# Kernel tuning notes

Hardware: AMD Instinct MI355X
Metric: run time of the kernel (lower is better)

Reference implementation:

```python
import jax, jax.numpy as jnp
import numpy as np

D_MODEL = 1024
NUM_HEADS = 16
D_K = D_MODEL // NUM_HEADS
B, N = 4, 2048


def setup_inputs() -> dict:
    key = jax.random.key(0)
    ks = jax.random.split(key, 5)
    scale = 1.0 / np.sqrt(D_MODEL)
    return {
        "x": jax.random.normal(ks[0], (B, N, D_MODEL), dtype=jnp.float32),
        "wq": jax.random.normal(ks[1], (D_MODEL, D_MODEL), dtype=jnp.float32) * scale,
        "wk": jax.random.normal(ks[2], (D_MODEL, D_MODEL), dtype=jnp.float32) * scale,
        "wv": jax.random.normal(ks[3], (D_MODEL, D_MODEL), dtype=jnp.float32) * scale,
        "wo": jax.random.normal(ks[4], (D_MODEL, D_MODEL), dtype=jnp.float32) * scale,
    }


def reference(x, wq, wk, wv, wo):
    b, n, d = x.shape
    # torch Linear(weight W) computes x @ W.T
    def proj(w):
        return (x @ w.T).reshape(b, n, NUM_HEADS, D_K).transpose(0, 2, 1, 3)  # [B,H,N,d_k]
    Q, K, V = proj(wq), proj(wk), proj(wv)
    scores = jnp.einsum("bhqd,bhkd->bhqk", Q, K) / jnp.sqrt(jnp.float32(D_K))
    causal = jnp.tril(jnp.ones((n, n), dtype=bool))
    scores = jnp.where(causal, scores, jnp.float32(-jnp.inf))
    attn = jax.nn.softmax(scores, axis=-1)
    vals = jnp.einsum("bhqk,bhkd->bhqd", attn, V)  # [B,H,N,d_k]
    vals = vals.transpose(0, 2, 1, 3).reshape(b, n, d)
    out = vals @ wo.T
    return (out, K, V)
```

## Files before the change

### kernel.cpp

```cpp
#include <hip/hip_runtime.h>
#include <hip/hip_bf16.h>

typedef __bf16 bf16_t;
typedef __bf16 bf16x8 __attribute__((ext_vector_type(8)));
typedef __bf16 bf16x4 __attribute__((ext_vector_type(4)));
typedef float f32x4 __attribute__((ext_vector_type(4)));
typedef float f32x16 __attribute__((ext_vector_type(16)));
typedef int i32x4 __attribute__((ext_vector_type(4)));

#define LDS_AS __attribute__((address_space(3)))
#define GLB_AS __attribute__((address_space(1)))

__device__ __forceinline__ void gload_lds16(const void* g, void* l) {
  __builtin_amdgcn_global_load_lds((const GLB_AS void*)g, (LDS_AS void*)l, 16, 0, 0);
}

static __device__ __forceinline__ f32x4 mfma16(bf16x8 a, bf16x8 b, f32x4 c) {
  return __builtin_amdgcn_mfma_f32_16x16x32_bf16(a, b, c, 0, 0, 0);
}
static __device__ __forceinline__ f32x16 mfma32(bf16x8 a, bf16x8 b, f32x16 c) {
  return __builtin_amdgcn_mfma_f32_32x32x16_bf16(a, b, c, 0, 0, 0);
}
__device__ __forceinline__ int cvtpk_bf16(float lo, float hi) {
  int r;
  asm("v_cvt_pk_bf16_f32 %0, %1, %2" : "=v"(r) : "v"(lo), "v"(hi));
  return r;
}
__device__ __forceinline__ bf16x8 mkfrag(int w0, int w1, int w2, int w3) {
  i32x4 v;
  v[0] = w0; v[1] = w1; v[2] = w2; v[3] = w3;
  return __builtin_bit_cast(bf16x8, v);
}

#define PIPE_WAIT_BARRIER(N)                                   \
  asm volatile("s_waitcnt vmcnt(" #N ")" ::: "memory");        \
  __builtin_amdgcn_s_barrier();                                \
  asm volatile("" ::: "memory");                               \
  __builtin_amdgcn_sched_barrier(0)

#define PIPE_END_BARRIER()                                     \
  __builtin_amdgcn_s_barrier();                                \
  asm volatile("" ::: "memory");                               \
  __builtin_amdgcn_sched_barrier(0)

#define QSCALE 0.18033688011112042f

__global__ __launch_bounds__(256) void cast_kernel(
    const float* __restrict__ x, const float* __restrict__ wq,
    const float* __restrict__ wk, const float* __restrict__ wv,
    const float* __restrict__ wo, bf16_t* __restrict__ xb,
    bf16_t* __restrict__ wqb, bf16_t* __restrict__ wkb,
    bf16_t* __restrict__ wvb, bf16_t* __restrict__ wob) {
  size_t i = ((size_t)blockIdx.x * 256 + threadIdx.x) * 4;
  const float* s;
  bf16_t* d;
  size_t off;
  if (i < 8388608) {
    s = x; d = xb; off = i;
  } else {
    size_t j = i - 8388608;
    int wi = (int)(j >> 20);
    off = j & 1048575;
    s = wi == 0 ? wq : wi == 1 ? wk : wi == 2 ? wv : wo;
    d = wi == 0 ? wqb : wi == 1 ? wkb : wi == 2 ? wvb : wob;
  }
  float4 v = *(const float4*)(s + off);
  bf16x4 o;
  o[0] = (bf16_t)v.x; o[1] = (bf16_t)v.y; o[2] = (bf16_t)v.z; o[3] = (bf16_t)v.w;
  *(bf16x4*)(d + off) = o;
}

__global__ __launch_bounds__(512) void gemm_qkv(
    const bf16_t* __restrict__ xb, const bf16_t* __restrict__ wqb,
    const bf16_t* __restrict__ wkb, const bf16_t* __restrict__ wvb,
    bf16_t* __restrict__ Qb, bf16_t* __restrict__ Kb, bf16_t* __restrict__ vTb,
    float* __restrict__ outK, float* __restrict__ outV) {
  __shared__ __align__(16) bf16_t lds[32768];
  const int tid = threadIdx.x;
  const int lane = tid & 63, w = tid >> 6;
  const int llo = lane & 15, lhi = lane >> 4;
  const int wm = w >> 2, wn = w & 3;
  const int rowBase = blockIdx.x * 128, colW = blockIdx.y * 128;

  const int arow = tid >> 2, asrc = (tid & 3) ^ ((arow >> 1) & 3);
  const bf16_t* srcA = xb + (size_t)(rowBase + arow) * 1024 + asrc * 8;
  const bf16_t* srcB0 = wqb + (size_t)(colW + arow) * 1024 + asrc * 8;
  const bf16_t* srcB1 = wkb + (size_t)(colW + arow) * 1024 + asrc * 8;
  const bf16_t* srcB2 = wvb + (size_t)(colW + arow) * 1024 + asrc * 8;
  const int dstA = tid * 8;
  const int dstB0 = 4096 + tid * 8;
  const int dstB1 = 4096 + (512 + tid) * 8;
  const int dstB2 = 4096 + (1024 + tid) * 8;

  auto STAGE = [&](int kt, int b) {
    bf16_t* base = lds + b * 16384;
    gload_lds16(srcA + kt * 32, base + dstA);
    gload_lds16(srcB0 + kt * 32, base + dstB0);
    gload_lds16(srcB1 + kt * 32, base + dstB1);
    gload_lds16(srcB2 + kt * 32, base + dstB2);
  };

  f32x4 acc[4][6] = {};
  const int xr = (llo >> 1) & 3;
  STAGE(0, 0);
  for (int kt = 0; kt < 32; ++kt) {
    if (kt + 1 < 32) {
      STAGE(kt + 1, (kt + 1) & 1);
      PIPE_WAIT_BARRIER(4);
    } else {
      PIPE_WAIT_BARRIER(0);
    }
    const bf16_t* bufA = lds + (kt & 1) * 16384;
    const bf16_t* bufB = bufA + 4096;
    bf16x8 aF[4], bF[6];
#pragma unroll
    for (int mf = 0; mf < 4; ++mf)
      aF[mf] = *(const bf16x8*)&bufA[(wm * 64 + mf * 16 + llo) * 32 +
                                     ((lhi ^ xr) * 8)];
#pragma unroll
    for (int nf = 0; nf < 6; ++nf)
      bF[nf] = *(const bf16x8*)&bufB[(wn * 96 + nf * 16 + llo) * 32 +
                                     ((lhi ^ xr) * 8)];
    __builtin_amdgcn_s_setprio(1);
#pragma unroll
    for (int mf = 0; mf < 4; ++mf)
#pragma unroll
      for (int nf = 0; nf < 6; ++nf) acc[mf][nf] = mfma16(aF[mf], bF[nf], acc[mf][nf]);
    __builtin_amdgcn_s_setprio(0);
    PIPE_END_BARRIER();
  }

#pragma unroll
  for (int mf = 0; mf < 4; ++mf) {
    int m0 = rowBase + wm * 64 + mf * 16 + lhi * 4;
    int b = m0 >> 11, tok0 = m0 & 2047;
#pragma unroll
    for (int nf = 0; nf < 6; ++nf) {
      int n = wn * 96 + nf * 16 + llo;
      int mat = n >> 7;
      int nm = colW + (n & 127);
      int h = nm >> 6, dk = nm & 63;
      size_t hoff = ((size_t)(b * 16 + h) * 2048 + tok0) * 64 + dk;
      if (mat == 0) {
#pragma unroll
        for (int r = 0; r < 4; ++r)
          Qb[hoff + (size_t)r * 64] = (bf16_t)(acc[mf][nf][r] * QSCALE);
      } else if (mat == 1) {
#pragma unroll
        for (int r = 0; r < 4; ++r) {
          outK[hoff + (size_t)r * 64] = acc[mf][nf][r];
          Kb[hoff + (size_t)r * 64] = (bf16_t)acc[mf][nf][r];
        }
      } else {
#pragma unroll
        for (int r = 0; r < 4; ++r) outV[hoff + (size_t)r * 64] = acc[mf][nf][r];
        bf16x4 pk;
#pragma unroll
        for (int r = 0; r < 4; ++r) pk[r] = (bf16_t)acc[mf][nf][r];
        *(bf16x4*)&vTb[((size_t)(b * 16 + h) * 64 + dk) * 2048 + tok0] = pk;
      }
    }
  }
}

__global__ __launch_bounds__(256) void gemm_out(const bf16_t* __restrict__ valsb,
                                                const bf16_t* __restrict__ wob,
                                                float* __restrict__ out) {
  __shared__ __align__(16) bf16_t lds[16384];
  const int tid = threadIdx.x;
  const int lane = tid & 63, w = tid >> 6;
  const int llo = lane & 15, lhi = lane >> 4;
  const int wm = w >> 1, wn = w & 1;
  const int rowBase = blockIdx.x * 128, colW = blockIdx.y * 128;

  int g0 = tid, g1 = 256 + tid;
  int r0 = g0 >> 2, r1 = g1 >> 2;
  int s0 = (g0 & 3) ^ ((r0 >> 1) & 3), s1 = (g1 & 3) ^ ((r1 >> 1) & 3);
  const bf16_t* srcA0 = valsb + (size_t)(rowBase + r0) * 1024 + s0 * 8;
  const bf16_t* srcA1 = valsb + (size_t)(rowBase + r1) * 1024 + s1 * 8;
  const bf16_t* srcB0 = wob + (size_t)(colW + r0) * 1024 + s0 * 8;
  const bf16_t* srcB1 = wob + (size_t)(colW + r1) * 1024 + s1 * 8;
  const int dA0 = g0 * 8, dA1 = g1 * 8;
  const int dB0 = 4096 + g0 * 8, dB1 = 4096 + g1 * 8;

  auto STAGE = [&](int kt, int b) {
    bf16_t* base = lds + b * 8192;
    gload_lds16(srcA0 + kt * 32, base + dA0);
    gload_lds16(srcA1 + kt * 32, base + dA1);
    gload_lds16(srcB0 + kt * 32, base + dB0);
    gload_lds16(srcB1 + kt * 32, base + dB1);
  };

  f32x4 acc[4][4] = {};
  const int xr = (llo >> 1) & 3;
  STAGE(0, 0);
  for (int kt = 0; kt < 32; ++kt) {
    if (kt + 1 < 32) {
      STAGE(kt + 1, (kt + 1) & 1);
      PIPE_WAIT_BARRIER(4);
    } else {
      PIPE_WAIT_BARRIER(0);
    }
    const bf16_t* bufA = lds + (kt & 1) * 8192;
    const bf16_t* bufB = bufA + 4096;
    bf16x8 aF[4], bF[4];
#pragma unroll
    for (int mf = 0; mf < 4; ++mf)
      aF[mf] = *(const bf16x8*)&bufA[(wm * 64 + mf * 16 + llo) * 32 +
                                     ((lhi ^ xr) * 8)];
#pragma unroll
    for (int nf = 0; nf < 4; ++nf)
      bF[nf] = *(const bf16x8*)&bufB[(wn * 64 + nf * 16 + llo) * 32 +
                                     ((lhi ^ xr) * 8)];
    __builtin_amdgcn_s_setprio(1);
#pragma unroll
    for (int mf = 0; mf < 4; ++mf)
#pragma unroll
      for (int nf = 0; nf < 4; ++nf) acc[mf][nf] = mfma16(aF[mf], bF[nf], acc[mf][nf]);
    __builtin_amdgcn_s_setprio(0);
    PIPE_END_BARRIER();
  }
#pragma unroll
  for (int mf = 0; mf < 4; ++mf) {
    int m0 = rowBase + wm * 64 + mf * 16 + lhi * 4;
#pragma unroll
    for (int nf = 0; nf < 4; ++nf) {
      int n = colW + wn * 64 + nf * 16 + llo;
#pragma unroll
      for (int r = 0; r < 4; ++r) out[(size_t)(m0 + r) * 1024 + n] = acc[mf][nf][r];
    }
  }
}

__global__ __launch_bounds__(256, 3) void attn_kernel(
    const bf16_t* __restrict__ Qb, const bf16_t* __restrict__ Kb,
    const bf16_t* __restrict__ vTb, bf16_t* __restrict__ valsb) {
  __shared__ bf16_t kS[2][64 * 64];
  __shared__ bf16_t vS[2][64 * 64];
  const int tid = threadIdx.x;
  const int w = tid >> 6, lane = tid & 63;
  const int ql = lane & 31, hi = lane >> 5, hi4 = hi * 4;
  const int head = blockIdx.x;
  const int qseg = 15 - blockIdx.y;
  const int qbase = qseg * 128;
  const int qw = qbase + w * 32;
  const int qrow = qw + ql;
  const int nkt = qseg * 2 + 2;
  const bf16_t* Qh = Qb + (size_t)head * 131072;
  const bf16_t* Kh = Kb + (size_t)head * 131072;
  const bf16_t* Vh = vTb + (size_t)head * 131072;

  bf16x8 qB[4];
#pragma unroll
  for (int kk = 0; kk < 4; ++kk)
    qB[kk] = *(const bf16x8*)&Qh[(size_t)qrow * 64 + kk * 16 + hi * 8];

  i32x4 ov;
  ov[0] = ov[1] = ov[2] = ov[3] = 0x3F803F80;
  const bf16x8 onesF = __builtin_bit_cast(bf16x8, ov);

  f32x16 oacc0 = {}, oacc1 = {};
  f32x16 lacc = {};

  const int c0 = tid, c1 = 256 + tid;
  const int r0 = c0 >> 3, r1 = c1 >> 3;
  const int s0 = (c0 & 7) ^ ((r0 ^ (r0 >> 3)) & 7);
  const int s1 = (c1 & 7) ^ ((r1 ^ (r1 >> 3)) & 7);

  auto STAGE = [&](int kt_, int bi) {
    const int kb_ = kt_ * 64;
    gload_lds16(Kh + (size_t)(kb_ + r0) * 64 + s0 * 8, &kS[bi][c0 * 8]);
    gload_lds16(Kh + (size_t)(kb_ + r1) * 64 + s1 * 8, &kS[bi][c1 * 8]);
    gload_lds16(Vh + (size_t)r0 * 2048 + kb_ + s0 * 8, &vS[bi][c0 * 8]);
    gload_lds16(Vh + (size_t)r1 * 2048 + kb_ + s1 * 8, &vS[bi][c1 * 8]);
  };

  const int swzA = (ql ^ (ql >> 3)) & 7;
  const int swzB = swzA ^ 4;

  STAGE(0, 0);
  __syncthreads();
  int cur = 0;
  for (int kt = 0; kt < nkt; ++kt) {
    const int kbase = kt * 64;
    if (kt + 1 < nkt) STAGE(kt + 1, cur ^ 1);
    if (kbase <= qw) {
      const bf16_t* kb = kS[cur];
      const bf16_t* vb = vS[cur];
      f32x16 st0 = {}, st1 = {};
      __builtin_amdgcn_s_setprio(1);
#pragma unroll
      for (int kk = 0; kk < 4; ++kk) {
        bf16x8 kf0 = *(const bf16x8*)&kb[ql * 64 + (((kk * 2 + hi) ^ swzA) * 8)];
        st0 = mfma32(kf0, qB[kk], st0);
      }
#pragma unroll
      for (int kk = 0; kk < 4; ++kk) {
        bf16x8 kf1 = *(const bf16x8*)&kb[(32 + ql) * 64 + (((kk * 2 + hi) ^ swzB) * 8)];
        st1 = mfma32(kf1, qB[kk], st1);
      }
      __builtin_amdgcn_s_setprio(0);
      if (kbase + 64 > qw) {
        const int lim = qrow - kbase;
#pragma unroll
        for (int rg = 0; rg < 16; ++rg) {
          const int kof = (rg & 3) + 8 * (rg >> 2) + hi4;
          if (kof > lim) st0[rg] = -__builtin_inff();
          if (kof + 32 > lim) st1[rg] = -__builtin_inff();
        }
      }
#pragma unroll
      for (int j = 0; j < 16; ++j) {
        st0[j] = __builtin_amdgcn_exp2f(st0[j]);
        st1[j] = __builtin_amdgcn_exp2f(st1[j]);
      }
      int a0 = cvtpk_bf16(st0[0], st0[1]), a1 = cvtpk_bf16(st0[2], st0[3]);
      int a2 = cvtpk_bf16(st0[4], st0[5]), a3 = cvtpk_bf16(st0[6], st0[7]);
      int a4 = cvtpk_bf16(st0[8], st0[9]), a5 = cvtpk_bf16(st0[10], st0[11]);
      int a6 = cvtpk_bf16(st0[12], st0[13]), a7 = cvtpk_bf16(st0[14], st0[15]);
      int b0 = cvtpk_bf16(st1[0], st1[1]), b1 = cvtpk_bf16(st1[2], st1[3]);
      int b2 = cvtpk_bf16(st1[4], st1[5]), b3 = cvtpk_bf16(st1[6], st1[7]);
      int b4 = cvtpk_bf16(st1[8], st1[9]), b5 = cvtpk_bf16(st1[10], st1[11]);
      int b6 = cvtpk_bf16(st1[12], st1[13]), b7 = cvtpk_bf16(st1[14], st1[15]);
      auto s02 = __builtin_amdgcn_permlane32_swap(a0, a2, false, false);
      auto s13 = __builtin_amdgcn_permlane32_swap(a1, a3, false, false);
      auto s46 = __builtin_amdgcn_permlane32_swap(a4, a6, false, false);
      auto s57 = __builtin_amdgcn_permlane32_swap(a5, a7, false, false);
      auto t02 = __builtin_amdgcn_permlane32_swap(b0, b2, false, false);
      auto t13 = __builtin_amdgcn_permlane32_swap(b1, b3, false, false);
      auto t46 = __builtin_amdgcn_permlane32_swap(b4, b6, false, false);
      auto t57 = __builtin_amdgcn_permlane32_swap(b5, b7, false, false);
      bf16x8 pB0 = mkfrag(s02[0], s13[0], s02[1], s13[1]);
      bf16x8 pB1 = mkfrag(s46[0], s57[0], s46[1], s57[1]);
      bf16x8 pB2 = mkfrag(t02[0], t13[0], t02[1], t13[1]);
      bf16x8 pB3 = mkfrag(t46[0], t57[0], t46[1], t57[1]);
      __builtin_amdgcn_s_setprio(1);
#pragma unroll
      for (int ks = 0; ks < 4; ++ks) {
        bf16x8 pb = ks == 0 ? pB0 : ks == 1 ? pB1 : ks == 2 ? pB2 : pB3;
        bf16x8 vf0 = *(const bf16x8*)&vb[ql * 64 + (((ks * 2 + hi) ^ swzA) * 8)];
        oacc0 = mfma32(vf0, pb, oacc0);
        bf16x8 vf1 = *(const bf16x8*)&vb[(32 + ql) * 64 + (((ks * 2 + hi) ^ swzB) * 8)];
        oacc1 = mfma32(vf1, pb, oacc1);
        lacc = mfma32(onesF, pb, lacc);
      }
      __builtin_amdgcn_s_setprio(0);
    }
    __syncthreads();
    cur ^= 1;
  }
  const float inv = 1.f / lacc[0];
  size_t base = ((size_t)(head >> 4) * 2048 + qrow) * 1024 + (head & 15) * 64 + hi4;
#pragma unroll
  for (int rg = 0; rg < 4; ++rg) {
    bf16x4 o0, o1;
#pragma unroll
    for (int j = 0; j < 4; ++j) {
      o0[j] = (bf16_t)(oacc0[rg * 4 + j] * inv);
      o1[j] = (bf16_t)(oacc1[rg * 4 + j] * inv);
    }
    *(bf16x4*)&valsb[base + rg * 8] = o0;
    *(bf16x4*)&valsb[base + 32 + rg * 8] = o1;
  }
}

extern "C" void kernel_launch(void* const* d_in, const int* in_sizes, int n_in,
                              void* d_out, int out_size, void* d_ws, size_t ws_size,
                              hipStream_t stream) {
  const float* x = (const float*)d_in[0];
  const float* wq = (const float*)d_in[1];
  const float* wk = (const float*)d_in[2];
  const float* wv = (const float*)d_in[3];
  const float* wo = (const float*)d_in[4];
  float* out = (float*)d_out;
  float* outK = out + 8388608;
  float* outV = out + 16777216;
  bf16_t* xb = (bf16_t*)d_ws;
  bf16_t* wqb = xb + 8388608;
  bf16_t* wkb = wqb + 1048576;
  bf16_t* wvb = wkb + 1048576;
  bf16_t* wob = wvb + 1048576;
  bf16_t* Qb = wob + 1048576;
  bf16_t* Kb = Qb + 8388608;
  bf16_t* vTb = Kb + 8388608;
  bf16_t* valsb = vTb + 8388608;
  cast_kernel<<<12288, 256, 0, stream>>>(x, wq, wk, wv, wo, xb, wqb, wkb, wvb, wob);
  gemm_qkv<<<dim3(64, 8), 512, 0, stream>>>(xb, wqb, wkb, wvb, Qb, Kb, vTb, outK, outV);
  attn_kernel<<<dim3(64, 16), 256, 0, stream>>>(Qb, Kb, vTb, valsb);
  gemm_out<<<dim3(64, 8), 256, 0, stream>>>(valsb, wob, out);
}
```

Before: 159.4 us.

## Remap QKV GEMM blocks per XCD and restructure its prefetch barrier

The QKV projection GEMM now launches as a 1D grid, and block indices are remapped so consecutive blocks on the same XCD cover the same row band. This is meant to improve L2 reuse of the activation tiles. The K-loop also changes its sync: it issues the next stage's loads, computes on the current buffer, then waits for all loads plus a barrier at the end of the iteration, instead of waiting before compute. That moves the load wait behind the MFMA work, though the full vmcnt(0) drain removes partial overlap. An LDS array in the output GEMM is renamed with no functional effect.

```diff
diff --git a/kernel.cpp b/kernel.cpp
--- a/kernel.cpp
+++ b/kernel.cpp
@@ -32,6 +32,12 @@
   return __builtin_bit_cast(bf16x8, v);
 }
 
+#define PIPE_TILE_END()                                        \
+  asm volatile("s_waitcnt vmcnt(0)" ::: "memory");             \
+  __builtin_amdgcn_s_barrier();                                \
+  asm volatile("" ::: "memory");                               \
+  __builtin_amdgcn_sched_barrier(0)
+
 #define PIPE_WAIT_BARRIER(N)                                   \
   asm volatile("s_waitcnt vmcnt(" #N ")" ::: "memory");        \
   __builtin_amdgcn_s_barrier();                                \
@@ -42,6 +48,12 @@
   __builtin_amdgcn_s_barrier();                                \
   asm volatile("" ::: "memory");                               \
   __builtin_amdgcn_sched_barrier(0)
+
+__device__ __forceinline__ void xcd_rc(int orig, int& rowI, int& colI) {
+  int logical = ((orig & 7) << 6) | (orig >> 3);
+  rowI = logical >> 3;
+  colI = logical & 7;
+}
 
 #define QSCALE 0.18033688011112042f
 
@@ -80,7 +92,9 @@
   const int lane = tid & 63, w = tid >> 6;
   const int llo = lane & 15, lhi = lane >> 4;
   const int wm = w >> 2, wn = w & 3;
-  const int rowBase = blockIdx.x * 128, colW = blockIdx.y * 128;
+  int rowI, colI;
+  xcd_rc(blockIdx.x, rowI, colI);
+  const int rowBase = rowI * 128, colW = colI * 128;
 
   const int arow = tid >> 2, asrc = (tid & 3) ^ ((arow >> 1) & 3);
   const bf16_t* srcA = xb + (size_t)(rowBase + arow) * 1024 + asrc * 8;
@@ -103,13 +117,10 @@
   f32x4 acc[4][6] = {};
   const int xr = (llo >> 1) & 3;
   STAGE(0, 0);
+  PIPE_TILE_END();
   for (int kt = 0; kt < 32; ++kt) {
-    if (kt + 1 < 32) {
-      STAGE(kt + 1, (kt + 1) & 1);
-      PIPE_WAIT_BARRIER(4);
-    } else {
-      PIPE_WAIT_BARRIER(0);
-    }
+    if (kt + 1 < 32) STAGE(kt + 1, (kt + 1) & 1);
+    __builtin_amdgcn_sched_barrier(0);
     const bf16_t* bufA = lds + (kt & 1) * 16384;
     const bf16_t* bufB = bufA + 4096;
     bf16x8 aF[4], bF[6];
@@ -127,7 +138,7 @@
 #pragma unroll
       for (int nf = 0; nf < 6; ++nf) acc[mf][nf] = mfma16(aF[mf], bF[nf], acc[mf][nf]);
     __builtin_amdgcn_s_setprio(0);
-    PIPE_END_BARRIER();
+    PIPE_TILE_END();
   }
 
 #pragma unroll
@@ -166,7 +177,7 @@
 __global__ __launch_bounds__(256) void gemm_out(const bf16_t* __restrict__ valsb,
                                                 const bf16_t* __restrict__ wob,
                                                 float* __restrict__ out) {
-  __shared__ __align__(16) bf16_t lds[16384];
+  __shared__ __align__(16) bf16_t slds[16384];
   const int tid = threadIdx.x;
   const int lane = tid & 63, w = tid >> 6;
   const int llo = lane & 15, lhi = lane >> 4;
@@ -184,7 +195,7 @@
   const int dB0 = 4096 + g0 * 8, dB1 = 4096 + g1 * 8;
 
   auto STAGE = [&](int kt, int b) {
-    bf16_t* base = lds + b * 8192;
+    bf16_t* base = slds + b * 8192;
     gload_lds16(srcA0 + kt * 32, base + dA0);
     gload_lds16(srcA1 + kt * 32, base + dA1);
     gload_lds16(srcB0 + kt * 32, base + dB0);
@@ -201,7 +212,7 @@
     } else {
       PIPE_WAIT_BARRIER(0);
     }
-    const bf16_t* bufA = lds + (kt & 1) * 8192;
+    const bf16_t* bufA = slds + (kt & 1) * 8192;
     const bf16_t* bufB = bufA + 4096;
     bf16x8 aF[4], bF[4];
 #pragma unroll
@@ -385,7 +396,7 @@
   bf16_t* vTb = Kb + 8388608;
   bf16_t* valsb = vTb + 8388608;
   cast_kernel<<<12288, 256, 0, stream>>>(x, wq, wk, wv, wo, xb, wqb, wkb, wvb, wob);
-  gemm_qkv<<<dim3(64, 8), 512, 0, stream>>>(xb, wqb, wkb, wvb, Qb, Kb, vTb, outK, outV);
+  gemm_qkv<<<512, 512, 0, stream>>>(xb, wqb, wkb, wvb, Qb, Kb, vTb, outK, outV);
   attn_kernel<<<dim3(64, 16), 256, 0, stream>>>(Qb, Kb, vTb, valsb);
   gemm_out<<<dim3(64, 8), 256, 0, stream>>>(valsb, wob, out);
 }
```

Result: no change. 161.5 us (+1.3%).
